# Kernel tuning notes

Measured on AMD Instinct MI355X. Metric: run time of the kernel, lower is better.

The kernel has to match this reference:

```python
import jax, jax.numpy as jnp
import numpy as np

ALPHA = 0.95   # membrane leak factor exp(-dt/tau_mem)
RHO   = 0.98   # threshold-adaptation decay
BETA  = 1.8    # adaptive threshold gain (ALIF)
TH0   = 1.0    # base threshold
SCALE = 10.0   # SuperSpike surrogate slope

@jax.custom_vjp
def spike(v):
    # Heaviside spike with SuperSpike surrogate gradient (as in cantata's SurrGradSpike)
    return (v >= 0.0).astype(v.dtype)

def _spike_fwd(v):
    return spike(v), v

def _spike_bwd(v, g):
    return (g / (SCALE * jnp.abs(v) + 1.0) ** 2,)

spike.defvjp(_spike_fwd, _spike_bwd)

def _onehot_delays(k, n, d):
    # each presynaptic source is routed through exactly one delay bin
    idx = jax.random.randint(k, (n,), 0, d)
    return (jnp.arange(d)[:, None] == idx[None, :]).astype(jnp.float32)  # [d, n]

def setup_inputs() -> dict:
    B, N, D, NE, DE = 32, 4096, 8, 2048, 4
    key = jax.random.key(0)
    ks = jax.random.split(key, 8)
    V = jax.random.normal(ks[0], (B, N), jnp.float32)
    a = jax.random.uniform(ks[1], (B, N), jnp.float32)
    Xd = (jax.random.uniform(ks[2], (D, B, N)) < 0.05).astype(jnp.float32)      # internal delay ring buffer
    Xext = (jax.random.uniform(ks[3], (DE, B, NE)) < 0.05).astype(jnp.float32)  # delayed external spikes
    W_int = jax.random.normal(ks[4], (N, N), jnp.float32) * 0.02
    W_ext = jax.random.normal(ks[5], (NE, N), jnp.float32) * 0.02
    dmap_int = _onehot_delays(ks[6], N, D)
    dmap_ext = _onehot_delays(ks[7], NE, DE)
    return dict(V=V, a=a, Xd=Xd, Xext=Xext, W_int=W_int, W_ext=W_ext,
                dmap_int=dmap_int, dmap_ext=dmap_ext)

def reference(V, a, Xd, Xext, W_int, W_ext, dmap_int, dmap_ext):
    # 1) ALIF spike generation from membrane + adaptive threshold
    th = TH0 + BETA * a
    X = spike(V - th)                                     # [B,N]
    a_new = RHO * a + X
    # 2) push new spikes into the delay ring buffer (delay 0 = current step)
    Xd_new = jnp.concatenate([X[None], Xd[:-1]], axis=0)  # [D,B,N]
    # 3) delay-mapped synaptic current: gather each presyn source from its delay bin,
    #    then dense delta-synapse accumulation (internal + cross-area)
    x_int = jnp.einsum('dbi,di->bi', Xd_new, dmap_int)    # [B,N]
    x_ext = jnp.einsum('dbi,di->bi', Xext, dmap_ext)      # [B,NE]
    current = x_int @ W_int + x_ext @ W_ext               # [B,N]
    # 4) membrane update: leak, reset on spike, integrate current
    V_new = ALPHA * V * (1.0 - X) + current
    return jnp.stack([X, V_new, a_new])                   # [3,B,N]
```

## Files before the change

kernel.cpp:

```cpp
#include <hip/hip_runtime.h>


#define B_   32
#define N_   4096
#define D_   8
#define NE_  2048
#define DE_  4
#define BN_  (B_ * N_)
#define BNE_ (B_ * NE_)

__global__ __launch_bounds__(256) void snn_spike_compact(
    const float* __restrict__ V, const float* __restrict__ a,
    const float* __restrict__ Xd, const float* __restrict__ Xext,
    const float* __restrict__ dmap_int, const float* __restrict__ dmap_ext,
    float* __restrict__ out, int* __restrict__ cnt,
    unsigned short* __restrict__ list_int, unsigned short* __restrict__ list_ext)
{
#pragma clang fp contract(off)
    __shared__ unsigned short s_i[512];
    __shared__ unsigned short s_e[256];
    __shared__ int lc_i, lc_e, base_i, base_e;
    int tid = threadIdx.x;
    if (tid == 0) { lc_i = 0; lc_e = 0; }
    __syncthreads();

    int b = blockIdx.y;
    int c = blockIdx.x;

    #pragma unroll
    for (int r = 0; r < 2; ++r) {
        int i = c * 512 + r * 256 + tid;
        int t = b * N_ + i;
        float av = a[t];
        float vv = V[t];
        float th = 1.0f + 1.8f * av;
        float x = (vv - th >= 0.0f) ? 1.0f : 0.0f;
        out[t] = x;
        out[2 * BN_ + t] = 0.98f * av + x;
        int di = 0;
        #pragma unroll
        for (int d = 1; d < D_; ++d)
            if (dmap_int[d * N_ + i] != 0.0f) di = d;
        float xi = (di == 0) ? x : Xd[(di - 1) * BN_ + t];
        if (xi != 0.0f) {
            int p = atomicAdd(&lc_i, 1);
            s_i[p] = (unsigned short)i;
        }
    }
    {
        int j = c * 256 + tid;
        int u = b * NE_ + j;
        int de = 0;
        #pragma unroll
        for (int d = 1; d < DE_; ++d)
            if (dmap_ext[d * NE_ + j] != 0.0f) de = d;
        float xe = Xext[de * BNE_ + u];
        if (xe != 0.0f) {
            int p = atomicAdd(&lc_e, 1);
            s_e[p] = (unsigned short)j;
        }
    }
    __syncthreads();
    if (tid == 0) {
        base_i = atomicAdd(&cnt[b], lc_i);
        base_e = atomicAdd(&cnt[B_ + b], lc_e);
    }
    __syncthreads();
    for (int k = tid; k < lc_i; k += 256) list_int[b * N_  + base_i + k] = s_i[k];
    for (int k = tid; k < lc_e; k += 256) list_ext[b * NE_ + base_e + k] = s_e[k];
}

__device__ __forceinline__ float4 ld4(const float* p) { return *(const float4*)p; }
__device__ __forceinline__ void add4(float4& a, const float4 w) {
    a.x += w.x; a.y += w.y; a.z += w.z; a.w += w.w;
}

__device__ __forceinline__ void accum_rows(const float* __restrict__ W,
                                           const unsigned short* sl, int n, int j,
                                           float4& acc)
{
    int nf = n & ~7;
    if (nf >= 8) {
        uint4 g = *(const uint4*)(sl);
        float4 p0 = ld4(W + (size_t)(g.x & 0xffff) * N_ + j);
        float4 p1 = ld4(W + (size_t)(g.x >> 16)    * N_ + j);
        float4 p2 = ld4(W + (size_t)(g.y & 0xffff) * N_ + j);
        float4 p3 = ld4(W + (size_t)(g.y >> 16)    * N_ + j);
        float4 p4 = ld4(W + (size_t)(g.z & 0xffff) * N_ + j);
        float4 p5 = ld4(W + (size_t)(g.z >> 16)    * N_ + j);
        float4 p6 = ld4(W + (size_t)(g.w & 0xffff) * N_ + j);
        float4 p7 = ld4(W + (size_t)(g.w >> 16)    * N_ + j);
        for (int k = 8; k < nf; k += 8) {
            uint4 g2 = *(const uint4*)(sl + k);
            float4 q0 = ld4(W + (size_t)(g2.x & 0xffff) * N_ + j);
            float4 q1 = ld4(W + (size_t)(g2.x >> 16)    * N_ + j);
            float4 q2 = ld4(W + (size_t)(g2.y & 0xffff) * N_ + j);
            float4 q3 = ld4(W + (size_t)(g2.y >> 16)    * N_ + j);
            float4 q4 = ld4(W + (size_t)(g2.z & 0xffff) * N_ + j);
            float4 q5 = ld4(W + (size_t)(g2.z >> 16)    * N_ + j);
            float4 q6 = ld4(W + (size_t)(g2.w & 0xffff) * N_ + j);
            float4 q7 = ld4(W + (size_t)(g2.w >> 16)    * N_ + j);
            add4(acc, p0); add4(acc, p1); add4(acc, p2); add4(acc, p3);
            add4(acc, p4); add4(acc, p5); add4(acc, p6); add4(acc, p7);
            p0 = q0; p1 = q1; p2 = q2; p3 = q3;
            p4 = q4; p5 = q5; p6 = q6; p7 = q7;
        }
        add4(acc, p0); add4(acc, p1); add4(acc, p2); add4(acc, p3);
        add4(acc, p4); add4(acc, p5); add4(acc, p6); add4(acc, p7);
    }
    for (int k = nf; k < n; ++k) {
        float4 w = ld4(W + (size_t)sl[k] * N_ + j);
        add4(acc, w);
    }
}

__global__ __launch_bounds__(64) void snn_current(
    const float* __restrict__ W_int, const float* __restrict__ W_ext,
    const float* __restrict__ V, float* __restrict__ out,
    const int* __restrict__ cnt,
    const unsigned short* __restrict__ list_int,
    const unsigned short* __restrict__ list_ext)
{
    __shared__ unsigned short s_int[N_];
    __shared__ unsigned short s_ext[NE_];
    int b = blockIdx.y;
    int ni = cnt[b];
    int ne = cnt[B_ + b];
    for (int k = threadIdx.x; k < ni; k += 64) s_int[k] = list_int[b * N_  + k];
    for (int k = threadIdx.x; k < ne; k += 64) s_ext[k] = list_ext[b * NE_ + k];
    __syncthreads();

    int j = blockIdx.x * 256 + threadIdx.x * 4;
    float4 acc = make_float4(0.f, 0.f, 0.f, 0.f);
    accum_rows(W_int, s_int, ni, j, acc);
    accum_rows(W_ext, s_ext, ne, j, acc);

    int t = b * N_ + j;
    float4 v = ld4(V + t);
    float4 x = ld4(out + t);
    float4 vn;
    vn.x = 0.95f * v.x * (1.0f - x.x) + acc.x;
    vn.y = 0.95f * v.y * (1.0f - x.y) + acc.y;
    vn.z = 0.95f * v.z * (1.0f - x.z) + acc.z;
    vn.w = 0.95f * v.w * (1.0f - x.w) + acc.w;
    *(float4*)(out + BN_ + t) = vn;
}

extern "C" void kernel_launch(void* const* d_in, const int* in_sizes, int n_in,
                              void* d_out, int out_size, void* d_ws, size_t ws_size,
                              hipStream_t stream)
{
    const float* V        = (const float*)d_in[0];
    const float* a        = (const float*)d_in[1];
    const float* Xd       = (const float*)d_in[2];
    const float* Xext     = (const float*)d_in[3];
    const float* W_int    = (const float*)d_in[4];
    const float* W_ext    = (const float*)d_in[5];
    const float* dmap_int = (const float*)d_in[6];
    const float* dmap_ext = (const float*)d_in[7];
    float* out = (float*)d_out;

    int* cnt = (int*)d_ws;
    unsigned short* list_int = (unsigned short*)((char*)d_ws + 256);
    unsigned short* list_ext = (unsigned short*)((char*)d_ws + 256 + (size_t)BN_ * 2);

    hipMemsetAsync(d_ws, 0, 256, stream);

    dim3 g1(8, 32);
    snn_spike_compact<<<g1, 256, 0, stream>>>(
        V, a, Xd, Xext, dmap_int, dmap_ext, out, cnt, list_int, list_ext);

    dim3 g2(16, 32);
    snn_current<<<g2, 64, 0, stream>>>(W_int, W_ext, V, out, cnt, list_int, list_ext);
}
```

Measured before the change: 149.8 us.

## Split spike-list accumulation across four waves and drop memset with per-chunk counts

The compaction kernel now writes a per-chunk spike count and list at a fixed offset instead of using global atomics. That removes the workspace memset launch and the second block-wide barrier. The current kernel grows from one wave to four per block: each wave sums a quarter of the active weight rows, and the partial sums are combined through shared memory. This adds in-flight memory loads for the latency-bound gather of W rows. The cost is an extra reduction step and a changed floating-point summation order.

After: 145.9 us. 1.03x faster.

```diff
diff --git a/kernel.cpp b/kernel.cpp
--- a/kernel.cpp
+++ b/kernel.cpp
@@ -8,18 +8,22 @@
 #define DE_  4
 #define BN_  (B_ * N_)
 #define BNE_ (B_ * NE_)
+#define NCH_ 8
+#define CI_  512
+#define CE_  256
 
 __global__ __launch_bounds__(256) void snn_spike_compact(
     const float* __restrict__ V, const float* __restrict__ a,
     const float* __restrict__ Xd, const float* __restrict__ Xext,
     const float* __restrict__ dmap_int, const float* __restrict__ dmap_ext,
-    float* __restrict__ out, int* __restrict__ cnt,
+    float* __restrict__ out,
+    int* __restrict__ cnt_int, int* __restrict__ cnt_ext,
     unsigned short* __restrict__ list_int, unsigned short* __restrict__ list_ext)
 {
 #pragma clang fp contract(off)
-    __shared__ unsigned short s_i[512];
-    __shared__ unsigned short s_e[256];
-    __shared__ int lc_i, lc_e, base_i, base_e;
+    __shared__ unsigned short s_i[CI_];
+    __shared__ unsigned short s_e[CE_];
+    __shared__ int lc_i, lc_e;
     int tid = threadIdx.x;
     if (tid == 0) { lc_i = 0; lc_e = 0; }
     __syncthreads();
@@ -29,7 +33,7 @@
 
     #pragma unroll
     for (int r = 0; r < 2; ++r) {
-        int i = c * 512 + r * 256 + tid;
+        int i = c * CI_ + r * 256 + tid;
         int t = b * N_ + i;
         float av = a[t];
         float vv = V[t];
@@ -48,7 +52,7 @@
         }
     }
     {
-        int j = c * 256 + tid;
+        int j = c * CE_ + tid;
         int u = b * NE_ + j;
         int de = 0;
         #pragma unroll
@@ -62,12 +66,11 @@
     }
     __syncthreads();
     if (tid == 0) {
-        base_i = atomicAdd(&cnt[b], lc_i);
-        base_e = atomicAdd(&cnt[B_ + b], lc_e);
-    }
-    __syncthreads();
-    for (int k = tid; k < lc_i; k += 256) list_int[b * N_  + base_i + k] = s_i[k];
-    for (int k = tid; k < lc_e; k += 256) list_ext[b * NE_ + base_e + k] = s_e[k];
+        cnt_int[b * NCH_ + c] = lc_i;
+        cnt_ext[b * NCH_ + c] = lc_e;
+    }
+    for (int k = tid; k < lc_i; k += 256) list_int[b * N_  + c * CI_ + k] = s_i[k];
+    for (int k = tid; k < lc_e; k += 256) list_ext[b * NE_ + c * CE_ + k] = s_e[k];
 }
 
 __device__ __forceinline__ float4 ld4(const float* p) { return *(const float4*)p; }
@@ -79,6 +82,7 @@
                                            const unsigned short* sl, int n, int j,
                                            float4& acc)
 {
+    if (n <= 0) return;
     int nf = n & ~7;
     if (nf >= 8) {
         uint4 g = *(const uint4*)(sl);
@@ -114,36 +118,64 @@
     }
 }
 
-__global__ __launch_bounds__(64) void snn_current(
+__global__ __launch_bounds__(256) void snn_current(
     const float* __restrict__ W_int, const float* __restrict__ W_ext,
     const float* __restrict__ V, float* __restrict__ out,
-    const int* __restrict__ cnt,
+    const int* __restrict__ cnt_int, const int* __restrict__ cnt_ext,
     const unsigned short* __restrict__ list_int,
     const unsigned short* __restrict__ list_ext)
 {
-    __shared__ unsigned short s_int[N_];
-    __shared__ unsigned short s_ext[NE_];
+    __shared__ __align__(16) unsigned short s_int[N_];
+    __shared__ __align__(16) unsigned short s_ext[NE_];
+    __shared__ float4 s_part[4][64];
+    int tid = threadIdx.x;
     int b = blockIdx.y;
-    int ni = cnt[b];
-    int ne = cnt[B_ + b];
-    for (int k = threadIdx.x; k < ni; k += 64) s_int[k] = list_int[b * N_  + k];
-    for (int k = threadIdx.x; k < ne; k += 64) s_ext[k] = list_ext[b * NE_ + k];
-    __syncthreads();
-
-    int j = blockIdx.x * 256 + threadIdx.x * 4;
+
+    int ci[NCH_], oi[NCH_], ce[NCH_], oe[NCH_];
+    int ni = 0, ne = 0;
+    #pragma unroll
+    for (int c = 0; c < NCH_; ++c) {
+        ci[c] = cnt_int[b * NCH_ + c]; oi[c] = ni; ni += ci[c];
+        ce[c] = cnt_ext[b * NCH_ + c]; oe[c] = ne; ne += ce[c];
+    }
+    #pragma unroll
+    for (int c = 0; c < NCH_; ++c) {
+        for (int k = tid; k < ci[c]; k += 256) s_int[oi[c] + k] = list_int[b * N_  + c * CI_ + k];
+        for (int k = tid; k < ce[c]; k += 256) s_ext[oe[c] + k] = list_ext[b * NE_ + c * CE_ + k];
+    }
+    __syncthreads();
+
+    int w = tid >> 6, lane = tid & 63;
+    int j = blockIdx.x * 256 + lane * 4;
     float4 acc = make_float4(0.f, 0.f, 0.f, 0.f);
-    accum_rows(W_int, s_int, ni, j, acc);
-    accum_rows(W_ext, s_ext, ne, j, acc);
-
-    int t = b * N_ + j;
-    float4 v = ld4(V + t);
-    float4 x = ld4(out + t);
-    float4 vn;
-    vn.x = 0.95f * v.x * (1.0f - x.x) + acc.x;
-    vn.y = 0.95f * v.y * (1.0f - x.y) + acc.y;
-    vn.z = 0.95f * v.z * (1.0f - x.z) + acc.z;
-    vn.w = 0.95f * v.w * (1.0f - x.w) + acc.w;
-    *(float4*)(out + BN_ + t) = vn;
+
+    int qi = ((ni + 31) >> 5) << 3;
+    int si = w * qi;
+    accum_rows(W_int, s_int + si, min(ni, si + qi) - si, j, acc);
+    int qe = ((ne + 31) >> 5) << 3;
+    int se = w * qe;
+    accum_rows(W_ext, s_ext + se, min(ne, se + qe) - se, j, acc);
+
+    s_part[w][lane] = acc;
+    __syncthreads();
+    if (w == 0) {
+        float4 a0 = s_part[0][lane], a1 = s_part[1][lane];
+        float4 a2 = s_part[2][lane], a3 = s_part[3][lane];
+        float4 cur;
+        cur.x = (a0.x + a1.x) + (a2.x + a3.x);
+        cur.y = (a0.y + a1.y) + (a2.y + a3.y);
+        cur.z = (a0.z + a1.z) + (a2.z + a3.z);
+        cur.w = (a0.w + a1.w) + (a2.w + a3.w);
+        int t = b * N_ + j;
+        float4 v = ld4(V + t);
+        float4 x = ld4(out + t);
+        float4 vn;
+        vn.x = 0.95f * v.x * (1.0f - x.x) + cur.x;
+        vn.y = 0.95f * v.y * (1.0f - x.y) + cur.y;
+        vn.z = 0.95f * v.z * (1.0f - x.z) + cur.z;
+        vn.w = 0.95f * v.w * (1.0f - x.w) + cur.w;
+        *(float4*)(out + BN_ + t) = vn;
+    }
 }
 
 extern "C" void kernel_launch(void* const* d_in, const int* in_sizes, int n_in,
@@ -160,16 +192,16 @@
     const float* dmap_ext = (const float*)d_in[7];
     float* out = (float*)d_out;
 
-    int* cnt = (int*)d_ws;
-    unsigned short* list_int = (unsigned short*)((char*)d_ws + 256);
-    unsigned short* list_ext = (unsigned short*)((char*)d_ws + 256 + (size_t)BN_ * 2);
-
-    hipMemsetAsync(d_ws, 0, 256, stream);
-
-    dim3 g1(8, 32);
+    int* cnt_int = (int*)d_ws;
+    int* cnt_ext = (int*)((char*)d_ws + 1024);
+    unsigned short* list_int = (unsigned short*)((char*)d_ws + 2048);
+    unsigned short* list_ext = (unsigned short*)((char*)d_ws + 2048 + (size_t)BN_ * 2);
+
+    dim3 g1(NCH_, B_);
     snn_spike_compact<<<g1, 256, 0, stream>>>(
-        V, a, Xd, Xext, dmap_int, dmap_ext, out, cnt, list_int, list_ext);
-
-    dim3 g2(16, 32);
-    snn_current<<<g2, 64, 0, stream>>>(W_int, W_ext, V, out, cnt, list_int, list_ext);
-}
+        V, a, Xd, Xext, dmap_int, dmap_ext, out, cnt_int, cnt_ext, list_int, list_ext);
+
+    dim3 g2(16, B_);
+    snn_current<<<g2, 256, 0, stream>>>(
+        W_int, W_ext, V, out, cnt_int, cnt_ext, list_int, list_ext);
+}
```
